# Kernel tuning notes

Measured on AMD Instinct MI355X. Metric: run time of the kernel, lower is better.

The kernel has to match this reference:

```python
import jax, jax.numpy as jnp
import numpy as np

T_STEPS = 64   # number of actions (T-1 in the torch code)
BATCH = 512
STATE = 256
ACTION = 64
BELIEF = 1024
HIDDEN = 1024
EMB = 1024
MIN_STD = 0.1


def setup_inputs() -> dict:
    key = jax.random.key(0)
    ks = jax.random.split(key, 16)
    def w(k, shape):
        return jax.random.normal(k, shape, jnp.float32) * 0.02
    return {
        "s_0": jax.random.normal(ks[0], (BATCH, STATE), jnp.float32),
        "A": jax.random.normal(ks[1], (T_STEPS, BATCH, ACTION), jnp.float32),
        "b_0": jax.random.normal(ks[2], (BATCH, BELIEF), jnp.float32),
        "O": jax.random.normal(ks[3], (T_STEPS, BATCH, EMB), jnp.float32),
        "M": jnp.ones((T_STEPS, BATCH, 1), jnp.float32),
        "noise_pri": jax.random.normal(ks[4], (T_STEPS, BATCH, STATE), jnp.float32),
        "noise_pos": jax.random.normal(ks[5], (T_STEPS, BATCH, STATE), jnp.float32),
        # learned parameters (torch nn.Linear convention: y = x @ W.T + b)
        "W_sa": w(ks[6], (BELIEF, STATE + ACTION)), "b_sa": jnp.zeros((BELIEF,), jnp.float32),
        "W_ih": w(ks[7], (3 * BELIEF, BELIEF)), "b_ih": jnp.zeros((3 * BELIEF,), jnp.float32),
        "W_hh": w(ks[8], (3 * BELIEF, BELIEF)), "b_hh": jnp.zeros((3 * BELIEF,), jnp.float32),
        "W_bpri": w(ks[9], (HIDDEN, BELIEF)), "b_bpri": jnp.zeros((HIDDEN,), jnp.float32),
        "W_spri": w(ks[10], (2 * STATE, HIDDEN)), "b_spri": jnp.zeros((2 * STATE,), jnp.float32),
        "W_bpos": w(ks[11], (HIDDEN, BELIEF + EMB)), "b_bpos": jnp.zeros((HIDDEN,), jnp.float32),
        "W_spos": w(ks[12], (2 * STATE, HIDDEN)), "b_spos": jnp.zeros((2 * STATE,), jnp.float32),
    }


def reference(s_0, A, b_0, O, M, noise_pri, noise_pos,
              W_sa, b_sa, W_ih, b_ih, W_hh, b_hh,
              W_bpri, b_bpri, W_spri, b_spri,
              W_bpos, b_bpos, W_spos, b_spos):
    act = jax.nn.relu  # cfg.activation_function = 'relu'

    def gru_cell(x, h):
        # torch GRUCell gate order: r, z, n
        gi = x @ W_ih.T + b_ih      # [B, 3*BELIEF]
        gh = h @ W_hh.T + b_hh
        i_r, i_z, i_n = jnp.split(gi, 3, axis=1)
        h_r, h_z, h_n = jnp.split(gh, 3, axis=1)
        r = jax.nn.sigmoid(i_r + h_r)
        z = jax.nn.sigmoid(i_z + h_z)
        n = jnp.tanh(i_n + r * h_n)
        return (1.0 - z) * n + z * h

    def step(carry, xs):
        b, s = carry  # belief [B,BELIEF], posterior state [B,STATE]
        a_t, o_t, m_t, eps_p, eps_q = xs
        s_in = s * m_t  # non-terminal mask
        x = act(jnp.concatenate([s_in, a_t], axis=1) @ W_sa.T + b_sa)
        b_new = gru_cell(x, b)
        # prior
        pri = act(b_new @ W_bpri.T + b_bpri) @ W_spri.T + b_spri
        mu_p, hp = jnp.split(pri, 2, axis=1)
        std_p = jax.nn.softplus(hp) + MIN_STD
        s_p = mu_p + std_p * eps_p
        # posterior (uses current observation embedding)
        pos = act(jnp.concatenate([b_new, o_t], axis=1) @ W_bpos.T + b_bpos) @ W_spos.T + b_spos
        mu_q, hq = jnp.split(pos, 2, axis=1)
        std_q = jax.nn.softplus(hq) + MIN_STD
        s_q = mu_q + std_q * eps_q
        return (b_new, s_q), (b_new, s_p, mu_p, std_p, s_q, mu_q, std_q)

    (_, _), ys = jax.lax.scan(step, (b_0, s_0), (A, O, M, noise_pri, noise_pos))
    B_out, S_pri, MU_pri, STD_pri, S_pos, MU_pos, STD_pos = ys
    return B_out, S_pri, MU_pri, STD_pri, S_pos, MU_pos, STD_pos
```

## Files before the change

kernel.cpp:

```cpp
#include <hip/hip_runtime.h>
#include <hip/hip_bf16.h>
#include <math.h>

typedef short bf16x8 __attribute__((ext_vector_type(8)));
typedef float f32x4 __attribute__((ext_vector_type(4)));
typedef unsigned short u16;

#define NT 64
#define NB 512
#define NS 256
#define NA 64
#define NBEL 1024

#define OUT_B      0
#define OUT_SPRI   33554432
#define OUT_MUPRI  41943040
#define OUT_STDPRI 50331648
#define OUT_SPOS   58720256
#define OUT_MUPOS  67108864
#define OUT_STDPOS 75497472

__device__ __forceinline__ f32x4 mfma16(bf16x8 a, bf16x8 b, f32x4 c) {
  return __builtin_amdgcn_mfma_f32_16x16x32_bf16(a, b, c, 0, 0, 0);
}

__device__ __forceinline__ u16 f2bf(float f) {
  union { float f; unsigned u; } v; v.f = f;
  return (u16)((v.u + 0x7FFFu + ((v.u >> 16) & 1u)) >> 16);
}
__device__ __forceinline__ float bf2f(u16 h) {
  union { unsigned u; float f; } v; v.u = ((unsigned)h) << 16; return v.f;
}

__device__ __forceinline__ bf16x8 ld8bf(const u16* p) { return *(const bf16x8*)p; }

__device__ __forceinline__ bf16x8 cvt8(const float* p) {
  const float4 lo = *(const float4*)p;
  const float4 hi = *(const float4*)(p + 4);
  bf16x8 v;
  v[0] = (short)f2bf(lo.x); v[1] = (short)f2bf(lo.y);
  v[2] = (short)f2bf(lo.z); v[3] = (short)f2bf(lo.w);
  v[4] = (short)f2bf(hi.x); v[5] = (short)f2bf(hi.y);
  v[6] = (short)f2bf(hi.z); v[7] = (short)f2bf(hi.w);
  return v;
}

__device__ __forceinline__ float sigm(float x) { return 1.f / (1.f + __expf(-x)); }
__device__ __forceinline__ float softplus_(float x) {
  if (x > 20.f) return x;
  return log1pf(__expf(x));
}

#define ZACC(acc) { acc[0][0] = (f32x4){0.f,0.f,0.f,0.f}; acc[0][1] = (f32x4){0.f,0.f,0.f,0.f}; \
                    acc[1][0] = (f32x4){0.f,0.f,0.f,0.f}; acc[1][1] = (f32x4){0.f,0.f,0.f,0.f}; }

#define Q4(acc, a0v, a1v, b0v, b1v) \
  acc[0][0] = mfma16(a0v, b0v, acc[0][0]); \
  acc[0][1] = mfma16(a0v, b1v, acc[0][1]); \
  acc[1][0] = mfma16(a1v, b0v, acc[1][0]); \
  acc[1][1] = mfma16(a1v, b1v, acc[1][1]);

__device__ __forceinline__ void gtile(f32x4 (&acc)[2][2],
    const u16* __restrict__ A, int lda, const u16* __restrict__ B, int ldb,
    int K, int r16, int kq) {
  const u16* A0 = A + r16 * lda + kq * 8;
  const u16* A1 = A0 + 16 * lda;
  const u16* B0 = B + (size_t)r16 * ldb + kq * 8;
  const u16* B1 = B0 + 16 * ldb;
#pragma unroll 4
  for (int k = 0; k < K; k += 32) {
    bf16x8 a0 = ld8bf(A0 + k), a1 = ld8bf(A1 + k);
    bf16x8 b0 = ld8bf(B0 + k), b1 = ld8bf(B1 + k);
    Q4(acc, a0, a1, b0, b1);
  }
}
__device__ __forceinline__ void gtileF(f32x4 (&acc)[2][2],
    const float* __restrict__ A, int lda, const u16* __restrict__ B, int ldb,
    int K, int r16, int kq) {
  const float* A0 = A + r16 * lda + kq * 8;
  const float* A1 = A0 + 16 * lda;
  const u16* B0 = B + (size_t)r16 * ldb + kq * 8;
  const u16* B1 = B0 + 16 * ldb;
#pragma unroll 2
  for (int k = 0; k < K; k += 32) {
    bf16x8 a0 = cvt8(A0 + k), a1 = cvt8(A1 + k);
    bf16x8 b0 = ld8bf(B0 + k), b1 = ld8bf(B1 + k);
    Q4(acc, a0, a1, b0, b1);
  }
}

__device__ __forceinline__ void red_write(float* L, f32x4 (&acc)[2][2], int l) {
  const int base = l * 16;
#pragma unroll
  for (int i = 0; i < 2; ++i)
#pragma unroll
    for (int j = 0; j < 2; ++j)
#pragma unroll
      for (int q = 0; q < 4; ++q)
        L[base + (i * 2 + j) * 4 + q] = acc[i][j][q];
}
__device__ __forceinline__ void red_add(const float* L, f32x4 (&acc)[2][2], int l) {
  const int base = l * 16;
#pragma unroll
  for (int i = 0; i < 2; ++i)
#pragma unroll
    for (int j = 0; j < 2; ++j)
#pragma unroll
      for (int q = 0; q < 4; ++q)
        acc[i][j][q] += L[base + (i * 2 + j) * 4 + q];
}

__device__ __forceinline__ void setflag_blk(unsigned* f) {
  __syncthreads();
  if (threadIdx.x == 0)
    __hip_atomic_fetch_add(f, 1u, __ATOMIC_RELEASE, __HIP_MEMORY_SCOPE_AGENT);
}
__device__ __forceinline__ void waitflag_blk(unsigned* f, unsigned target) {
  if (threadIdx.x == 0) {
    while (__hip_atomic_load(f, __ATOMIC_RELAXED, __HIP_MEMORY_SCOPE_AGENT) < target)
      __builtin_amdgcn_s_sleep(2);
    (void)__hip_atomic_load(f, __ATOMIC_ACQUIRE, __HIP_MEMORY_SCOPE_AGENT);
  }
  __syncthreads();
}

__global__ __launch_bounds__(256) void cvt_weights_k(
    const float* __restrict__ wsa, const float* __restrict__ wih,
    const float* __restrict__ whh, const float* __restrict__ wbpri,
    const float* __restrict__ wspri, const float* __restrict__ wbpos,
    const float* __restrict__ wspos, u16* __restrict__ dst) {
  const int S0 = 327680;
  const int S1 = S0 + 3145728;
  const int S2 = S1 + 3145728;
  const int S3 = S2 + 1048576;
  const int S4 = S3 + 524288;
  const int S5 = S4 + 2097152;
  const int S6 = S5 + 524288;
  for (int i = blockIdx.x * blockDim.x + threadIdx.x; i < S6;
       i += gridDim.x * blockDim.x) {
    float v;
    if (i < S0) v = wsa[i];
    else if (i < S1) v = wih[i - S0];
    else if (i < S2) v = whh[i - S1];
    else if (i < S3) v = wbpri[i - S2];
    else if (i < S4) v = wspri[i - S3];
    else if (i < S5) v = wbpos[i - S4];
    else v = wspos[i - S5];
    dst[i] = f2bf(v);
  }
}

__global__ __launch_bounds__(256) void init_carry_k(
    const float* __restrict__ s0, const float* __restrict__ b0,
    const float* __restrict__ Mptr, u16* __restrict__ smask,
    u16* __restrict__ bbf, float* __restrict__ hf,
    unsigned* __restrict__ flags) {
  for (int i = blockIdx.x * blockDim.x + threadIdx.x; i < NB * NBEL;
       i += gridDim.x * blockDim.x) {
    float b = b0[i];
    bbf[i] = f2bf(b);
    hf[i] = b;
    if (i < NB * NS) {
      int row = i >> 8;
      smask[i] = f2bf(s0[i] * Mptr[row]);
    }
    if (i < 3 * NT) flags[i] = 0;
  }
}


__device__ __forceinline__ void dev_spri(
    int g, int wid, int kh, int r16, int kq, int l, int tt,
    const u16* __restrict__ hpri, const u16* __restrict__ wspri,
    const float* __restrict__ bspri, const float* __restrict__ npri,
    float* __restrict__ out, float* lred0, float* lred1) {
  const int bm = g >> 2, bn = g & 3;
  const int row0 = bm * 64 + (wid >> 1) * 32;
  const int c0 = bn * 64 + (wid & 1) * 32;
  f32x4 am[2][2], ah[2][2];
  ZACC(am); ZACC(ah);
  const u16* A0 = hpri + (row0 + r16) * NBEL + kh * 512 + kq * 8;
  const u16* A1 = A0 + 16 * NBEL;
  const u16* Bm0 = wspri + (size_t)(c0 + r16) * NBEL + kh * 512 + kq * 8;
  const u16* Bm1 = Bm0 + 16 * NBEL;
  const u16* Bh0 = wspri + (size_t)(c0 + 256 + r16) * NBEL + kh * 512 + kq * 8;
  const u16* Bh1 = Bh0 + 16 * NBEL;
#pragma unroll 4
  for (int k = 0; k < 512; k += 32) {
    bf16x8 a0 = ld8bf(A0 + k), a1 = ld8bf(A1 + k);
    bf16x8 m0 = ld8bf(Bm0 + k), m1 = ld8bf(Bm1 + k);
    Q4(am, a0, a1, m0, m1);
    bf16x8 h0 = ld8bf(Bh0 + k), h1 = ld8bf(Bh1 + k);
    Q4(ah, a0, a1, h0, h1);
  }
  if (kh == 1) {
    red_write(lred0, am, l);
    red_write(lred1, ah, l);
  }
  __syncthreads();
  if (kh == 0) {
    red_add(lred0, am, l);
    red_add(lred1, ah, l);
#pragma unroll
    for (int i = 0; i < 2; ++i)
#pragma unroll
      for (int j = 0; j < 2; ++j)
#pragma unroll
        for (int q = 0; q < 4; ++q) {
          const int row = row0 + i * 16 + kq * 4 + q;
          const int c = c0 + j * 16 + r16;
          const size_t idx = (size_t)tt * (NB * NS) + (size_t)row * NS + c;
          const float mu = am[i][j][q] + bspri[c];
          const float hp = ah[i][j][q] + bspri[c + 256];
          const float sd = softplus_(hp) + 0.1f;
          out[OUT_SPRI + idx] = mu + sd * npri[idx];
          out[OUT_MUPRI + idx] = mu;
          out[OUT_STDPRI + idx] = sd;
        }
  }
}

__device__ __forceinline__ void dev_x64(
    int g, int wid8, int r16, int kq, int t,
    const u16* __restrict__ smask, const float* __restrict__ Af,
    const u16* __restrict__ wsa, const float* __restrict__ bsa,
    u16* __restrict__ xg) {
  const int row0 = (g >> 3) * 64 + (wid8 >> 2) * 32;
  const int col0 = (g & 7) * 128 + (wid8 & 3) * 32;
  f32x4 acc[2][2]; ZACC(acc);
  gtile(acc, smask + row0 * NS, NS, wsa + (size_t)col0 * 320, 320, 256, r16, kq);
  gtileF(acc, Af + (size_t)t * (NB * NA) + (size_t)row0 * NA, NA,
         wsa + (size_t)col0 * 320 + 256, 320, 64, r16, kq);
#pragma unroll
  for (int i = 0; i < 2; ++i)
#pragma unroll
    for (int j = 0; j < 2; ++j)
#pragma unroll
      for (int q = 0; q < 4; ++q) {
        const int row = row0 + i * 16 + kq * 4 + q;
        const int col = col0 + j * 16 + r16;
        xg[row * NBEL + col] = f2bf(fmaxf(acc[i][j][q] + bsa[col], 0.f));
      }
}

__device__ __forceinline__ void dev_hbO64(
    int g, int wid8, int r16, int kq,
    const float* __restrict__ OfT, const u16* __restrict__ wbpos,
    float* __restrict__ hbOn) {
  const int row0 = (g >> 3) * 64 + (wid8 >> 2) * 32;
  const int col0 = (g & 7) * 128 + (wid8 & 3) * 32;
  f32x4 acc[2][2]; ZACC(acc);
  gtileF(acc, OfT + (size_t)row0 * NBEL, NBEL,
         wbpos + (size_t)col0 * 2048 + 1024, 2048, 1024, r16, kq);
#pragma unroll
  for (int i = 0; i < 2; ++i)
#pragma unroll
    for (int j = 0; j < 2; ++j)
#pragma unroll
      for (int q = 0; q < 4; ++q) {
        const int row = row0 + i * 16 + kq * 4 + q;
        const int col = col0 + j * 16 + r16;
        hbOn[row * NBEL + col] = acc[i][j][q];
      }
}

__device__ __forceinline__ void dev_gh96(
    int g, int wid8, int r16, int kq,
    const u16* __restrict__ bsrc, const u16* __restrict__ whh,
    const float* __restrict__ bhh, u16* __restrict__ ghn) {
  const int bm = g / 12, bc = g % 12;
  const int row0 = bm * 64 + (wid8 >> 2) * 32;
#pragma unroll
  for (int jt = 0; jt < 2; ++jt) {
    const int col0 = bc * 256 + (wid8 & 3) * 32 + jt * 128;
    f32x4 acc[2][2]; ZACC(acc);
    gtile(acc, bsrc + row0 * NBEL, NBEL, whh + (size_t)col0 * NBEL, NBEL,
          1024, r16, kq);
#pragma unroll
    for (int i = 0; i < 2; ++i)
#pragma unroll
      for (int j = 0; j < 2; ++j)
#pragma unroll
        for (int q = 0; q < 4; ++q) {
          const int row = row0 + i * 16 + kq * 4 + q;
          const int col = col0 + j * 16 + r16;
          ghn[row * 3072 + col] = f2bf(acc[i][j][q] + bhh[col]);
        }
  }
}

__device__ __forceinline__ void dev_bpri64(
    int g, int wid8, int r16, int kq,
    const u16* __restrict__ bcur, const u16* __restrict__ wbpri,
    const float* __restrict__ bbpri, u16* __restrict__ hpri) {
  const int row0 = (g >> 3) * 64 + (wid8 >> 2) * 32;
  const int col0 = (g & 7) * 128 + (wid8 & 3) * 32;
  f32x4 acc[2][2]; ZACC(acc);
  gtile(acc, bcur + row0 * NBEL, NBEL, wbpri + (size_t)col0 * NBEL, NBEL,
        1024, r16, kq);
#pragma unroll
  for (int i = 0; i < 2; ++i)
#pragma unroll
    for (int j = 0; j < 2; ++j)
#pragma unroll
      for (int q = 0; q < 4; ++q) {
        const int row = row0 + i * 16 + kq * 4 + q;
        const int col = col0 + j * 16 + r16;
        hpri[row * NBEL + col] = f2bf(fmaxf(acc[i][j][q] + bbpri[col], 0.f));
      }
}

__global__ __launch_bounds__(512, 2) void kX0(
    const u16* __restrict__ smask, const float* __restrict__ Af,
    const u16* __restrict__ wsa, const float* __restrict__ bsa,
    u16* __restrict__ xg, const float* __restrict__ Of,
    const u16* __restrict__ wbpos, float* __restrict__ hbO0,
    const u16* __restrict__ bbf, const u16* __restrict__ whh,
    const float* __restrict__ bhh, u16* __restrict__ ghA) {
  const int l = threadIdx.x & 63, r16 = l & 15, kq = l >> 4;
  const int wid8 = threadIdx.x >> 6;
  if (blockIdx.x < 64) {
    dev_x64(blockIdx.x, wid8, r16, kq, 0, smask, Af, wsa, bsa, xg);
  } else if (blockIdx.x < 128) {
    dev_hbO64(blockIdx.x - 64, wid8, r16, kq, Of, wbpos, hbO0);
  } else {
    dev_gh96(blockIdx.x - 128, wid8, r16, kq, bbf, whh, bhh, ghA);
  }
}

__global__ __launch_bounds__(512, 2) void kG(
    const u16* __restrict__ xg, const u16* __restrict__ wih,
    const float* __restrict__ bih, const u16* __restrict__ ghc,
    float* __restrict__ hf, u16* __restrict__ bcur, float* __restrict__ out,
    const u16* __restrict__ hpri, const u16* __restrict__ wspri,
    const float* __restrict__ bspri, const float* __restrict__ npri, int t) {
  __shared__ float lred[4][3][1024];
  const int l = threadIdx.x & 63, r16 = l & 15, kq = l >> 4;
  const int wid8 = threadIdx.x >> 6;
  const int wid = wid8 & 3, kh = wid8 >> 2;
  if (blockIdx.x < 128) {
    const int g = blockIdx.x, bm = g >> 4, bn = g & 15;
    const int row0 = bm * 64 + (wid >> 1) * 32;
    const int col0 = bn * 64 + (wid & 1) * 32;
    f32x4 ar[2][2], az[2][2], an[2][2];
    ZACC(ar); ZACC(az); ZACC(an);
    const u16* A0 = xg + (row0 + r16) * NBEL + kh * 512 + kq * 8;
    const u16* A1 = A0 + 16 * NBEL;
    const u16* Br0 = wih + (size_t)(col0 + r16) * NBEL + kh * 512 + kq * 8;
    const u16* Br1 = Br0 + 16 * NBEL;
    const u16* Bz0 = wih + (size_t)(col0 + 1024 + r16) * NBEL + kh * 512 + kq * 8;
    const u16* Bz1 = Bz0 + 16 * NBEL;
    const u16* Bn0 = wih + (size_t)(col0 + 2048 + r16) * NBEL + kh * 512 + kq * 8;
    const u16* Bn1 = Bn0 + 16 * NBEL;
#pragma unroll 4
    for (int k = 0; k < 512; k += 32) {
      bf16x8 a0 = ld8bf(A0 + k), a1 = ld8bf(A1 + k);
      bf16x8 b0 = ld8bf(Br0 + k), b1 = ld8bf(Br1 + k);
      Q4(ar, a0, a1, b0, b1);
      bf16x8 c0 = ld8bf(Bz0 + k), c1 = ld8bf(Bz1 + k);
      Q4(az, a0, a1, c0, c1);
      bf16x8 d0 = ld8bf(Bn0 + k), d1 = ld8bf(Bn1 + k);
      Q4(an, a0, a1, d0, d1);
    }
    if (kh == 1) {
      red_write(&lred[wid][0][0], ar, l);
      red_write(&lred[wid][1][0], az, l);
      red_write(&lred[wid][2][0], an, l);
    }
    __syncthreads();
    if (kh == 0) {
      const int base = l * 16;
#pragma unroll
      for (int i = 0; i < 2; ++i)
#pragma unroll
        for (int j = 0; j < 2; ++j)
#pragma unroll
          for (int q = 0; q < 4; ++q) {
            const int row = row0 + i * 16 + kq * 4 + q;
            const int c = col0 + j * 16 + r16;
            const int li = base + (i * 2 + j) * 4 + q;
            const u16* ghrow = ghc + row * 3072;
            const float r = sigm(ar[i][j][q] + lred[wid][0][li] + bih[c] +
                                 bf2f(ghrow[c]));
            const float z = sigm(az[i][j][q] + lred[wid][1][li] + bih[c + 1024] +
                                 bf2f(ghrow[c + 1024]));
            const float n = tanhf(an[i][j][q] + lred[wid][2][li] + bih[c + 2048] +
                                  r * bf2f(ghrow[c + 2048]));
            const float h = hf[row * NBEL + c];
            const float bnew = (1.f - z) * n + z * h;
            hf[row * NBEL + c] = bnew;
            bcur[row * NBEL + c] = f2bf(bnew);
            out[OUT_B + (size_t)t * (NB * NBEL) + row * NBEL + c] = bnew;
          }
    }
  } else if (t >= 1) {
    dev_spri(blockIdx.x - 128, wid, kh, r16, kq, l, t - 1,
             hpri, wspri, bspri, npri, out,
             &lred[wid][0][0], &lred[wid][1][0]);
  }
}

__global__ __launch_bounds__(512, 2) void kM(
    const u16* __restrict__ bcur, const u16* __restrict__ wbpos,
    const float* __restrict__ bbpos, const float* __restrict__ hbOc,
    u16* __restrict__ hbbf,
    const u16* __restrict__ wbpri, const float* __restrict__ bbpri,
    u16* __restrict__ hpri,
    const u16* __restrict__ whh, const float* __restrict__ bhh,
    u16* __restrict__ ghn,
    const float* __restrict__ Of, float* __restrict__ hbOn,
    const u16* __restrict__ wspos, const float* __restrict__ bspos,
    const float* __restrict__ npos, const float* __restrict__ Mptr,
    u16* __restrict__ smask,
    const float* __restrict__ Af, const u16* __restrict__ wsa,
    const float* __restrict__ bsa, u16* __restrict__ xg,
    const u16* __restrict__ wspri, const float* __restrict__ bspri,
    const float* __restrict__ npri,
    float* __restrict__ out,
    unsigned* __restrict__ fH, unsigned* __restrict__ fS,
    unsigned* __restrict__ fB, int t) {
  __shared__ float lred[4][2][1024];
  const int l = threadIdx.x & 63, r16 = l & 15, kq = l >> 4;
  const int wid8 = threadIdx.x >> 6;
  const int wid = wid8 & 3, kh = wid8 >> 2;
  if (blockIdx.x < 128) {
    const int g = blockIdx.x, bm = g >> 4, bn = g & 15;
    const int row0 = bm * 64 + (wid >> 1) * 32;
    const int col0 = bn * 64 + (wid & 1) * 32;
    f32x4 acc[2][2]; ZACC(acc);
    const u16* A0 = bcur + (row0 + r16) * NBEL + kh * 512 + kq * 8;
    const u16* A1 = A0 + 16 * NBEL;
    const u16* B0 = wbpos + (size_t)(col0 + r16) * 2048 + kh * 512 + kq * 8;
    const u16* B1 = B0 + 16 * 2048;
#pragma unroll 4
    for (int k = 0; k < 512; k += 32) {
      bf16x8 a0 = ld8bf(A0 + k), a1 = ld8bf(A1 + k);
      bf16x8 b0 = ld8bf(B0 + k), b1 = ld8bf(B1 + k);
      Q4(acc, a0, a1, b0, b1);
    }
    if (kh == 1) red_write(&lred[wid][0][0], acc, l);
    __syncthreads();
    if (kh == 0) {
      red_add(&lred[wid][0][0], acc, l);
#pragma unroll
      for (int i = 0; i < 2; ++i)
#pragma unroll
        for (int j = 0; j < 2; ++j)
#pragma unroll
          for (int q = 0; q < 4; ++q) {
            const int row = row0 + i * 16 + kq * 4 + q;
            const int col = col0 + j * 16 + r16;
            const float v = acc[i][j][q] + hbOc[row * NBEL + col] + bbpos[col];
            hbbf[row * NBEL + col] = f2bf(fmaxf(v, 0.f));
          }
    }
    setflag_blk(&fH[t]);
  } else if (blockIdx.x < 192) {
    dev_bpri64(blockIdx.x - 128, wid8, r16, kq, bcur, wbpri, bbpri, hpri);
    setflag_blk(&fB[t]);
  } else if (blockIdx.x < 288) {
    if (t + 1 >= NT) return;
    dev_gh96(blockIdx.x - 192, wid8, r16, kq, bcur, whh, bhh, ghn);
  } else if (blockIdx.x < 352) {
    if (t + 1 >= NT) return;
    dev_hbO64(blockIdx.x - 288, wid8, r16, kq,
              Of + (size_t)(t + 1) * (NB * NBEL), wbpos, hbOn);
  } else if (blockIdx.x < 384) {
    waitflag_blk(&fH[t], 128);
    const int g = blockIdx.x - 352, bm = g >> 2, bn = g & 3;
    const int row0 = bm * 64 + (wid >> 1) * 32;
    const int c0 = bn * 64 + (wid & 1) * 32;
    f32x4 am[2][2], ah[2][2];
    ZACC(am); ZACC(ah);
    const u16* A0 = hbbf + (row0 + r16) * NBEL + kh * 512 + kq * 8;
    const u16* A1 = A0 + 16 * NBEL;
    const u16* Bm0 = wspos + (size_t)(c0 + r16) * NBEL + kh * 512 + kq * 8;
    const u16* Bm1 = Bm0 + 16 * NBEL;
    const u16* Bh0 = wspos + (size_t)(c0 + 256 + r16) * NBEL + kh * 512 + kq * 8;
    const u16* Bh1 = Bh0 + 16 * NBEL;
#pragma unroll 4
    for (int k = 0; k < 512; k += 32) {
      bf16x8 a0 = ld8bf(A0 + k), a1 = ld8bf(A1 + k);
      bf16x8 m0 = ld8bf(Bm0 + k), m1 = ld8bf(Bm1 + k);
      Q4(am, a0, a1, m0, m1);
      bf16x8 h0 = ld8bf(Bh0 + k), h1 = ld8bf(Bh1 + k);
      Q4(ah, a0, a1, h0, h1);
    }
    if (kh == 1) {
      red_write(&lred[wid][0][0], am, l);
      red_write(&lred[wid][1][0], ah, l);
    }
    __syncthreads();
    if (kh == 0) {
      red_add(&lred[wid][0][0], am, l);
      red_add(&lred[wid][1][0], ah, l);
#pragma unroll
      for (int i = 0; i < 2; ++i)
#pragma unroll
        for (int j = 0; j < 2; ++j)
#pragma unroll
          for (int q = 0; q < 4; ++q) {
            const int row = row0 + i * 16 + kq * 4 + q;
            const int c = c0 + j * 16 + r16;
            const float mu = am[i][j][q] + bspos[c];
            const float hq = ah[i][j][q] + bspos[c + 256];
            const float sd = softplus_(hq) + 0.1f;
            const size_t idx = (size_t)t * (NB * NS) + (size_t)row * NS + c;
            const float sq = mu + sd * npos[idx];
            out[OUT_SPOS + idx] = sq;
            out[OUT_MUPOS + idx] = mu;
            out[OUT_STDPOS + idx] = sd;
            const float mn = (t < NT - 1) ? Mptr[(t + 1) * NB + row] : 1.f;
            smask[row * NS + c] = f2bf(sq * mn);
          }
    }
    setflag_blk(&fS[t]);
  } else if (blockIdx.x < 448) {
    if (t + 1 >= NT) return;
    waitflag_blk(&fS[t], 32);
    dev_x64(blockIdx.x - 384, wid8, r16, kq, t + 1, smask, Af, wsa, bsa, xg);
  } else {
    if (t != NT - 1) return;
    waitflag_blk(&fB[t], 64);
    dev_spri(blockIdx.x - 448, wid, kh, r16, kq, l, t,
             hpri, wspri, bspri, npri, out,
             &lred[wid][0][0], &lred[wid][1][0]);
  }
}

extern "C" void kernel_launch(void* const* d_in, const int* in_sizes, int n_in,
                              void* d_out, int out_size, void* d_ws, size_t ws_size,
                              hipStream_t stream) {
  const float* s0 = (const float*)d_in[0];
  const float* Af = (const float*)d_in[1];
  const float* b0 = (const float*)d_in[2];
  const float* Of = (const float*)d_in[3];
  const float* Mp = (const float*)d_in[4];
  const float* npri = (const float*)d_in[5];
  const float* npos = (const float*)d_in[6];
  const float* Wsa = (const float*)d_in[7];
  const float* bsa = (const float*)d_in[8];
  const float* Wih = (const float*)d_in[9];
  const float* bih = (const float*)d_in[10];
  const float* Whh = (const float*)d_in[11];
  const float* bhh = (const float*)d_in[12];
  const float* Wbpri = (const float*)d_in[13];
  const float* bbpri = (const float*)d_in[14];
  const float* Wspri = (const float*)d_in[15];
  const float* bspri = (const float*)d_in[16];
  const float* Wbpos = (const float*)d_in[17];
  const float* bbpos = (const float*)d_in[18];
  const float* Wspos = (const float*)d_in[19];
  const float* bspos = (const float*)d_in[20];

  float* out = (float*)d_out;
  char* ws = (char*)d_ws;
  u16* wbase   = (u16*)ws;
  u16* wsa_b   = wbase;
  u16* wih_b   = wbase + 327680;
  u16* whh_b   = wbase + 3473408;
  u16* wbpri_b = wbase + 6619136;
  u16* wspri_b = wbase + 7667712;
  u16* wbpos_b = wbase + 8192000;
  u16* wspos_b = wbase + 10289152;
  u16*   smask = (u16*)  (ws + 21626880);
  u16*   bbf   = (u16*)  (ws + 21889024);
  float* hf    = (float*)(ws + 22937600);
  u16*   xg    = (u16*)  (ws + 25034752);
  float* hbO0  = (float*)(ws + 26083328);
  float* hbO1  = (float*)(ws + 28180480);
  u16*   hbbf  = (u16*)  (ws + 30277632);
  u16*   hpri  = (u16*)  (ws + 31326208);
  u16*   ghA   = (u16*)  (ws + 32374784);
  u16*   ghB   = (u16*)  (ws + 35520512);
  unsigned* flags = (unsigned*)(ws + 38666240);
  unsigned* fH = flags, *fS = flags + NT, *fB = flags + 2 * NT;

  cvt_weights_k<<<2048, 256, 0, stream>>>(Wsa, Wih, Whh, Wbpri, Wspri, Wbpos,
                                          Wspos, wbase);
  init_carry_k<<<2048, 256, 0, stream>>>(s0, b0, Mp, smask, bbf, hf, flags);
  kX0<<<224, 512, 0, stream>>>(smask, Af, wsa_b, bsa, xg, Of, wbpos_b, hbO0,
                               bbf, whh_b, bhh, ghA);

  for (int t = 0; t < NT; ++t) {
    float* hbOc = (t & 1) ? hbO1 : hbO0;
    float* hbOn = (t & 1) ? hbO0 : hbO1;
    u16* ghc = (t & 1) ? ghB : ghA;
    u16* ghn = (t & 1) ? ghA : ghB;
    kG<<<160, 512, 0, stream>>>(xg, wih_b, bih, ghc, hf, bbf, out,
                                hpri, wspri_b, bspri, npri, t);
    kM<<<480, 512, 0, stream>>>(bbf, wbpos_b, bbpos, hbOc, hbbf,
                                wbpri_b, bbpri, hpri,
                                whh_b, bhh, ghn,
                                Of, hbOn,
                                wspos_b, bspos, npos, Mp, smask,
                                Af, wsa_b, bsa, xg,
                                wspri_b, bspri, npri,
                                out, fH, fS, fB, t);
  }
}
```

Baseline: 8.208 ms.

## Merge per-step GRU and head kernels into one flag-synchronized kernel

Folds the two per-timestep launches (GRU gate kernel and the multi-stage head kernel) into a single 496-block launch. Blocks coordinate through global flags: a new GRU-done flag gates the posterior, prior-hidden and next-step W_hh projections. The prior-hidden buffer is double-buffered so the delayed prior-state head can read the previous step while the current one is written. The W_hh, prior-hidden and observation-projection stages now run on fewer, larger blocks to fit the combined grid. This removes one launch boundary per step and lets independent stages overlap with the GRU tail, at the cost of spin-waiting blocks that rely on every block being resident at once.

```diff
diff --git a/kernel.cpp b/kernel.cpp
--- a/kernel.cpp
+++ b/kernel.cpp
@@ -164,7 +164,7 @@
       int row = i >> 8;
       smask[i] = f2bf(s0[i] * Mptr[row]);
     }
-    if (i < 3 * NT) flags[i] = 0;
+    if (i < 4 * NT) flags[i] = 0;
   }
 }
 
@@ -264,6 +264,30 @@
       }
 }
 
+__device__ __forceinline__ void dev_hbO32(
+    int g, int wid8, int r16, int kq,
+    const float* __restrict__ OfT, const u16* __restrict__ wbpos,
+    float* __restrict__ hbOn) {
+  const int row0 = (g >> 2) * 64 + (wid8 >> 2) * 32;
+#pragma unroll
+  for (int jt = 0; jt < 2; ++jt) {
+    const int col0 = (g & 3) * 256 + jt * 128 + (wid8 & 3) * 32;
+    f32x4 acc[2][2]; ZACC(acc);
+    gtileF(acc, OfT + (size_t)row0 * NBEL, NBEL,
+           wbpos + (size_t)col0 * 2048 + 1024, 2048, 1024, r16, kq);
+#pragma unroll
+    for (int i = 0; i < 2; ++i)
+#pragma unroll
+      for (int j = 0; j < 2; ++j)
+#pragma unroll
+        for (int q = 0; q < 4; ++q) {
+          const int row = row0 + i * 16 + kq * 4 + q;
+          const int col = col0 + j * 16 + r16;
+          hbOn[row * NBEL + col] = acc[i][j][q];
+        }
+  }
+}
+
 __device__ __forceinline__ void dev_gh96(
     int g, int wid8, int r16, int kq,
     const u16* __restrict__ bsrc, const u16* __restrict__ whh,
@@ -289,25 +313,53 @@
   }
 }
 
-__device__ __forceinline__ void dev_bpri64(
+__device__ __forceinline__ void dev_gh48(
+    int g, int wid8, int r16, int kq,
+    const u16* __restrict__ bsrc, const u16* __restrict__ whh,
+    const float* __restrict__ bhh, u16* __restrict__ ghn) {
+  const int bm = g / 6, bc = g % 6;
+  const int row0 = bm * 64 + (wid8 >> 2) * 32;
+#pragma unroll
+  for (int jt = 0; jt < 4; ++jt) {
+    const int col0 = bc * 512 + jt * 128 + (wid8 & 3) * 32;
+    f32x4 acc[2][2]; ZACC(acc);
+    gtile(acc, bsrc + row0 * NBEL, NBEL, whh + (size_t)col0 * NBEL, NBEL,
+          1024, r16, kq);
+#pragma unroll
+    for (int i = 0; i < 2; ++i)
+#pragma unroll
+      for (int j = 0; j < 2; ++j)
+#pragma unroll
+        for (int q = 0; q < 4; ++q) {
+          const int row = row0 + i * 16 + kq * 4 + q;
+          const int col = col0 + j * 16 + r16;
+          ghn[row * 3072 + col] = f2bf(acc[i][j][q] + bhh[col]);
+        }
+  }
+}
+
+__device__ __forceinline__ void dev_bpri32(
     int g, int wid8, int r16, int kq,
     const u16* __restrict__ bcur, const u16* __restrict__ wbpri,
     const float* __restrict__ bbpri, u16* __restrict__ hpri) {
-  const int row0 = (g >> 3) * 64 + (wid8 >> 2) * 32;
-  const int col0 = (g & 7) * 128 + (wid8 & 3) * 32;
-  f32x4 acc[2][2]; ZACC(acc);
-  gtile(acc, bcur + row0 * NBEL, NBEL, wbpri + (size_t)col0 * NBEL, NBEL,
-        1024, r16, kq);
-#pragma unroll
-  for (int i = 0; i < 2; ++i)
-#pragma unroll
-    for (int j = 0; j < 2; ++j)
-#pragma unroll
-      for (int q = 0; q < 4; ++q) {
-        const int row = row0 + i * 16 + kq * 4 + q;
-        const int col = col0 + j * 16 + r16;
-        hpri[row * NBEL + col] = f2bf(fmaxf(acc[i][j][q] + bbpri[col], 0.f));
-      }
+  const int row0 = (g >> 2) * 64 + (wid8 >> 2) * 32;
+#pragma unroll
+  for (int jt = 0; jt < 2; ++jt) {
+    const int col0 = (g & 3) * 256 + jt * 128 + (wid8 & 3) * 32;
+    f32x4 acc[2][2]; ZACC(acc);
+    gtile(acc, bcur + row0 * NBEL, NBEL, wbpri + (size_t)col0 * NBEL, NBEL,
+          1024, r16, kq);
+#pragma unroll
+    for (int i = 0; i < 2; ++i)
+#pragma unroll
+      for (int j = 0; j < 2; ++j)
+#pragma unroll
+        for (int q = 0; q < 4; ++q) {
+          const int row = row0 + i * 16 + kq * 4 + q;
+          const int col = col0 + j * 16 + r16;
+          hpri[row * NBEL + col] = f2bf(fmaxf(acc[i][j][q] + bbpri[col], 0.f));
+        }
+  }
 }
 
 __global__ __launch_bounds__(512, 2) void kX0(
@@ -328,12 +380,26 @@
   }
 }
 
-__global__ __launch_bounds__(512, 2) void kG(
+__global__ __launch_bounds__(512, 2) void kS(
     const u16* __restrict__ xg, const u16* __restrict__ wih,
     const float* __restrict__ bih, const u16* __restrict__ ghc,
-    float* __restrict__ hf, u16* __restrict__ bcur, float* __restrict__ out,
-    const u16* __restrict__ hpri, const u16* __restrict__ wspri,
-    const float* __restrict__ bspri, const float* __restrict__ npri, int t) {
+    float* __restrict__ hf, u16* __restrict__ bbf, float* __restrict__ out,
+    const u16* __restrict__ hpriPrev, u16* __restrict__ hpriCur,
+    const u16* __restrict__ wspri, const float* __restrict__ bspri,
+    const float* __restrict__ npri,
+    const u16* __restrict__ wbpos, const float* __restrict__ bbpos,
+    const float* __restrict__ hbOc, u16* __restrict__ hbbf,
+    const u16* __restrict__ wbpri, const float* __restrict__ bbpri,
+    const u16* __restrict__ whh, const float* __restrict__ bhh,
+    u16* __restrict__ ghn,
+    const float* __restrict__ Of, float* __restrict__ hbOn,
+    const u16* __restrict__ wspos, const float* __restrict__ bspos,
+    const float* __restrict__ npos, const float* __restrict__ Mptr,
+    u16* __restrict__ smask,
+    const float* __restrict__ Af, const u16* __restrict__ wsa,
+    const float* __restrict__ bsa,
+    unsigned* __restrict__ fG, unsigned* __restrict__ fH,
+    unsigned* __restrict__ fS, unsigned* __restrict__ fB, int t) {
   __shared__ float lred[4][3][1024];
   const int l = threadIdx.x & 63, r16 = l & 15, kq = l >> 4;
   const int wid8 = threadIdx.x >> 6;
@@ -389,46 +455,23 @@
             const float h = hf[row * NBEL + c];
             const float bnew = (1.f - z) * n + z * h;
             hf[row * NBEL + c] = bnew;
-            bcur[row * NBEL + c] = f2bf(bnew);
+            bbf[row * NBEL + c] = f2bf(bnew);
             out[OUT_B + (size_t)t * (NB * NBEL) + row * NBEL + c] = bnew;
           }
     }
-  } else if (t >= 1) {
-    dev_spri(blockIdx.x - 128, wid, kh, r16, kq, l, t - 1,
-             hpri, wspri, bspri, npri, out,
-             &lred[wid][0][0], &lred[wid][1][0]);
-  }
-}
-
-__global__ __launch_bounds__(512, 2) void kM(
-    const u16* __restrict__ bcur, const u16* __restrict__ wbpos,
-    const float* __restrict__ bbpos, const float* __restrict__ hbOc,
-    u16* __restrict__ hbbf,
-    const u16* __restrict__ wbpri, const float* __restrict__ bbpri,
-    u16* __restrict__ hpri,
-    const u16* __restrict__ whh, const float* __restrict__ bhh,
-    u16* __restrict__ ghn,
-    const float* __restrict__ Of, float* __restrict__ hbOn,
-    const u16* __restrict__ wspos, const float* __restrict__ bspos,
-    const float* __restrict__ npos, const float* __restrict__ Mptr,
-    u16* __restrict__ smask,
-    const float* __restrict__ Af, const u16* __restrict__ wsa,
-    const float* __restrict__ bsa, u16* __restrict__ xg,
-    const u16* __restrict__ wspri, const float* __restrict__ bspri,
-    const float* __restrict__ npri,
-    float* __restrict__ out,
-    unsigned* __restrict__ fH, unsigned* __restrict__ fS,
-    unsigned* __restrict__ fB, int t) {
-  __shared__ float lred[4][2][1024];
-  const int l = threadIdx.x & 63, r16 = l & 15, kq = l >> 4;
-  const int wid8 = threadIdx.x >> 6;
-  const int wid = wid8 & 3, kh = wid8 >> 2;
-  if (blockIdx.x < 128) {
-    const int g = blockIdx.x, bm = g >> 4, bn = g & 15;
+    setflag_blk(fG + t);
+  } else if (blockIdx.x < 160) {
+    if (t >= 1)
+      dev_spri(blockIdx.x - 128, wid, kh, r16, kq, l, t - 1,
+               hpriPrev, wspri, bspri, npri, out,
+               &lred[wid][0][0], &lred[wid][1][0]);
+  } else if (blockIdx.x < 288) {
+    waitflag_blk(fG + t, 128);
+    const int g = blockIdx.x - 160, bm = g >> 4, bn = g & 15;
     const int row0 = bm * 64 + (wid >> 1) * 32;
     const int col0 = bn * 64 + (wid & 1) * 32;
     f32x4 acc[2][2]; ZACC(acc);
-    const u16* A0 = bcur + (row0 + r16) * NBEL + kh * 512 + kq * 8;
+    const u16* A0 = bbf + (row0 + r16) * NBEL + kh * 512 + kq * 8;
     const u16* A1 = A0 + 16 * NBEL;
     const u16* B0 = wbpos + (size_t)(col0 + r16) * 2048 + kh * 512 + kq * 8;
     const u16* B1 = B0 + 16 * 2048;
@@ -454,20 +497,23 @@
             hbbf[row * NBEL + col] = f2bf(fmaxf(v, 0.f));
           }
     }
-    setflag_blk(&fH[t]);
-  } else if (blockIdx.x < 192) {
-    dev_bpri64(blockIdx.x - 128, wid8, r16, kq, bcur, wbpri, bbpri, hpri);
-    setflag_blk(&fB[t]);
-  } else if (blockIdx.x < 288) {
-    if (t + 1 >= NT) return;
-    dev_gh96(blockIdx.x - 192, wid8, r16, kq, bcur, whh, bhh, ghn);
-  } else if (blockIdx.x < 352) {
-    if (t + 1 >= NT) return;
-    dev_hbO64(blockIdx.x - 288, wid8, r16, kq,
-              Of + (size_t)(t + 1) * (NB * NBEL), wbpos, hbOn);
-  } else if (blockIdx.x < 384) {
-    waitflag_blk(&fH[t], 128);
-    const int g = blockIdx.x - 352, bm = g >> 2, bn = g & 3;
+    setflag_blk(fH + t);
+  } else if (blockIdx.x < 320) {
+    waitflag_blk(fG + t, 128);
+    dev_bpri32(blockIdx.x - 288, wid8, r16, kq, bbf, wbpri, bbpri, hpriCur);
+    setflag_blk(fB + t);
+  } else if (blockIdx.x < 368) {
+    if (t + 1 < NT) {
+      waitflag_blk(fG + t, 128);
+      dev_gh48(blockIdx.x - 320, wid8, r16, kq, bbf, whh, bhh, ghn);
+    }
+  } else if (blockIdx.x < 400) {
+    if (t + 1 < NT)
+      dev_hbO32(blockIdx.x - 368, wid8, r16, kq,
+                Of + (size_t)(t + 1) * (NB * NBEL), wbpos, hbOn);
+  } else if (blockIdx.x < 432) {
+    waitflag_blk(fH + t, 128);
+    const int g = blockIdx.x - 400, bm = g >> 2, bn = g & 3;
     const int row0 = bm * 64 + (wid >> 1) * 32;
     const int c0 = bn * 64 + (wid & 1) * 32;
     f32x4 am[2][2], ah[2][2];
@@ -514,17 +560,18 @@
             smask[row * NS + c] = f2bf(sq * mn);
           }
     }
-    setflag_blk(&fS[t]);
-  } else if (blockIdx.x < 448) {
-    if (t + 1 >= NT) return;
-    waitflag_blk(&fS[t], 32);
-    dev_x64(blockIdx.x - 384, wid8, r16, kq, t + 1, smask, Af, wsa, bsa, xg);
+    setflag_blk(fS + t);
   } else {
-    if (t != NT - 1) return;
-    waitflag_blk(&fB[t], 64);
-    dev_spri(blockIdx.x - 448, wid, kh, r16, kq, l, t,
-             hpri, wspri, bspri, npri, out,
-             &lred[wid][0][0], &lred[wid][1][0]);
+    if (t + 1 < NT) {
+      waitflag_blk(fS + t, 32);
+      dev_x64(blockIdx.x - 432, wid8, r16, kq, t + 1, smask, Af, wsa, bsa,
+              (u16*)xg);
+    } else if (blockIdx.x < 464) {
+      waitflag_blk(fB + t, 32);
+      dev_spri(blockIdx.x - 432, wid, kh, r16, kq, l, t,
+               hpriCur, wspri, bspri, npri, out,
+               &lred[wid][0][0], &lred[wid][1][0]);
+    }
   }
 }
 
@@ -570,11 +617,13 @@
   float* hbO0  = (float*)(ws + 26083328);
   float* hbO1  = (float*)(ws + 28180480);
   u16*   hbbf  = (u16*)  (ws + 30277632);
-  u16*   hpri  = (u16*)  (ws + 31326208);
-  u16*   ghA   = (u16*)  (ws + 32374784);
-  u16*   ghB   = (u16*)  (ws + 35520512);
-  unsigned* flags = (unsigned*)(ws + 38666240);
-  unsigned* fH = flags, *fS = flags + NT, *fB = flags + 2 * NT;
+  u16*   hpri0 = (u16*)  (ws + 31326208);
+  u16*   hpri1 = (u16*)  (ws + 32374784);
+  u16*   ghA   = (u16*)  (ws + 33423360);
+  u16*   ghB   = (u16*)  (ws + 36569088);
+  unsigned* flags = (unsigned*)(ws + 39714816);
+  unsigned* fG = flags, *fH = flags + NT, *fS = flags + 2 * NT,
+          *fB = flags + 3 * NT;
 
   cvt_weights_k<<<2048, 256, 0, stream>>>(Wsa, Wih, Whh, Wbpri, Wspri, Wbpos,
                                           Wspos, wbase);
@@ -587,15 +636,16 @@
     float* hbOn = (t & 1) ? hbO0 : hbO1;
     u16* ghc = (t & 1) ? ghB : ghA;
     u16* ghn = (t & 1) ? ghA : ghB;
-    kG<<<160, 512, 0, stream>>>(xg, wih_b, bih, ghc, hf, bbf, out,
-                                hpri, wspri_b, bspri, npri, t);
-    kM<<<480, 512, 0, stream>>>(bbf, wbpos_b, bbpos, hbOc, hbbf,
-                                wbpri_b, bbpri, hpri,
+    u16* hpriCur  = (t & 1) ? hpri1 : hpri0;
+    u16* hpriPrev = (t & 1) ? hpri0 : hpri1;
+    kS<<<496, 512, 0, stream>>>(xg, wih_b, bih, ghc, hf, bbf, out,
+                                hpriPrev, hpriCur, wspri_b, bspri, npri,
+                                wbpos_b, bbpos, hbOc, hbbf,
+                                wbpri_b, bbpri,
                                 whh_b, bhh, ghn,
                                 Of, hbOn,
                                 wspos_b, bspos, npos, Mp, smask,
-                                Af, wsa_b, bsa, xg,
-                                wspri_b, bspri, npri,
-                                out, fH, fS, fB, t);
-  }
-}
+                                Af, wsa_b, bsa,
+                                fG, fH, fS, fB, t);
+  }
+}
```

Result: slower. 14.18 ms (+72.8%).

## Move next-step obs projection into GRU kernel and use per-row-block flags

Applied to the files above, without the earlier changes.

The O_{t+1}·W_bpos projection for the next step moves from the kM kernel into the kG kernel as extra blocks, so it runs alongside the GRU gate GEMM. kM shrinks from 480 to 416 blocks. The single global flags become per-row-block flags, so each posterior block waits only for its 16 producer blocks and each x-projection block waits only for its 4. The prior hidden buffer is double-buffered so kG at step t can read step t-1's hpri while kM writes the new one. The aim is to fill idle CUs in the underoccupied kG launch and to cut spin-wait latency, at the cost of more grid blocks and more flag bookkeeping.

```diff
diff --git a/kernel.cpp b/kernel.cpp
--- a/kernel.cpp
+++ b/kernel.cpp
@@ -164,7 +164,7 @@
       int row = i >> 8;
       smask[i] = f2bf(s0[i] * Mptr[row]);
     }
-    if (i < 3 * NT) flags[i] = 0;
+    if (i < 2048) flags[i] = 0;
   }
 }
 
@@ -332,8 +332,10 @@
     const u16* __restrict__ xg, const u16* __restrict__ wih,
     const float* __restrict__ bih, const u16* __restrict__ ghc,
     float* __restrict__ hf, u16* __restrict__ bcur, float* __restrict__ out,
-    const u16* __restrict__ hpri, const u16* __restrict__ wspri,
-    const float* __restrict__ bspri, const float* __restrict__ npri, int t) {
+    const u16* __restrict__ hpriPrev, const u16* __restrict__ wspri,
+    const float* __restrict__ bspri, const float* __restrict__ npri,
+    const float* __restrict__ Of, const u16* __restrict__ wbpos,
+    float* __restrict__ hbOn, int t) {
   __shared__ float lred[4][3][1024];
   const int l = threadIdx.x & 63, r16 = l & 15, kq = l >> 4;
   const int wid8 = threadIdx.x >> 6;
@@ -393,10 +395,15 @@
             out[OUT_B + (size_t)t * (NB * NBEL) + row * NBEL + c] = bnew;
           }
     }
-  } else if (t >= 1) {
-    dev_spri(blockIdx.x - 128, wid, kh, r16, kq, l, t - 1,
-             hpri, wspri, bspri, npri, out,
-             &lred[wid][0][0], &lred[wid][1][0]);
+  } else if (blockIdx.x < 160) {
+    if (t >= 1)
+      dev_spri(blockIdx.x - 128, wid, kh, r16, kq, l, t - 1,
+               hpriPrev, wspri, bspri, npri, out,
+               &lred[wid][0][0], &lred[wid][1][0]);
+  } else {
+    if (t + 1 < NT)
+      dev_hbO64(blockIdx.x - 160, wid8, r16, kq,
+                Of + (size_t)(t + 1) * (NB * NBEL), wbpos, hbOn);
   }
 }
 
@@ -405,10 +412,9 @@
     const float* __restrict__ bbpos, const float* __restrict__ hbOc,
     u16* __restrict__ hbbf,
     const u16* __restrict__ wbpri, const float* __restrict__ bbpri,
-    u16* __restrict__ hpri,
+    u16* __restrict__ hpriCur,
     const u16* __restrict__ whh, const float* __restrict__ bhh,
     u16* __restrict__ ghn,
-    const float* __restrict__ Of, float* __restrict__ hbOn,
     const u16* __restrict__ wspos, const float* __restrict__ bspos,
     const float* __restrict__ npos, const float* __restrict__ Mptr,
     u16* __restrict__ smask,
@@ -417,7 +423,7 @@
     const u16* __restrict__ wspri, const float* __restrict__ bspri,
     const float* __restrict__ npri,
     float* __restrict__ out,
-    unsigned* __restrict__ fH, unsigned* __restrict__ fS,
+    unsigned* __restrict__ fH8, unsigned* __restrict__ fS8,
     unsigned* __restrict__ fB, int t) {
   __shared__ float lred[4][2][1024];
   const int l = threadIdx.x & 63, r16 = l & 15, kq = l >> 4;
@@ -454,20 +460,16 @@
             hbbf[row * NBEL + col] = f2bf(fmaxf(v, 0.f));
           }
     }
-    setflag_blk(&fH[t]);
+    setflag_blk(fH8 + t * 8 + bm);
   } else if (blockIdx.x < 192) {
-    dev_bpri64(blockIdx.x - 128, wid8, r16, kq, bcur, wbpri, bbpri, hpri);
-    setflag_blk(&fB[t]);
+    dev_bpri64(blockIdx.x - 128, wid8, r16, kq, bcur, wbpri, bbpri, hpriCur);
+    setflag_blk(fB + t);
   } else if (blockIdx.x < 288) {
-    if (t + 1 >= NT) return;
-    dev_gh96(blockIdx.x - 192, wid8, r16, kq, bcur, whh, bhh, ghn);
-  } else if (blockIdx.x < 352) {
-    if (t + 1 >= NT) return;
-    dev_hbO64(blockIdx.x - 288, wid8, r16, kq,
-              Of + (size_t)(t + 1) * (NB * NBEL), wbpos, hbOn);
-  } else if (blockIdx.x < 384) {
-    waitflag_blk(&fH[t], 128);
-    const int g = blockIdx.x - 352, bm = g >> 2, bn = g & 3;
+    if (t + 1 < NT)
+      dev_gh96(blockIdx.x - 192, wid8, r16, kq, bcur, whh, bhh, ghn);
+  } else if (blockIdx.x < 320) {
+    const int g = blockIdx.x - 288, bm = g >> 2, bn = g & 3;
+    waitflag_blk(fH8 + t * 8 + bm, 16);
     const int row0 = bm * 64 + (wid >> 1) * 32;
     const int c0 = bn * 64 + (wid & 1) * 32;
     f32x4 am[2][2], ah[2][2];
@@ -514,16 +516,17 @@
             smask[row * NS + c] = f2bf(sq * mn);
           }
     }
-    setflag_blk(&fS[t]);
-  } else if (blockIdx.x < 448) {
+    setflag_blk(fS8 + t * 8 + bm);
+  } else if (blockIdx.x < 384) {
     if (t + 1 >= NT) return;
-    waitflag_blk(&fS[t], 32);
-    dev_x64(blockIdx.x - 384, wid8, r16, kq, t + 1, smask, Af, wsa, bsa, xg);
+    const int g = blockIdx.x - 320;
+    waitflag_blk(fS8 + t * 8 + (g >> 3), 4);
+    dev_x64(g, wid8, r16, kq, t + 1, smask, Af, wsa, bsa, xg);
   } else {
     if (t != NT - 1) return;
-    waitflag_blk(&fB[t], 64);
-    dev_spri(blockIdx.x - 448, wid, kh, r16, kq, l, t,
-             hpri, wspri, bspri, npri, out,
+    waitflag_blk(fB + t, 64);
+    dev_spri(blockIdx.x - 384, wid, kh, r16, kq, l, t,
+             hpriCur, wspri, bspri, npri, out,
              &lred[wid][0][0], &lred[wid][1][0]);
   }
 }
@@ -570,11 +573,14 @@
   float* hbO0  = (float*)(ws + 26083328);
   float* hbO1  = (float*)(ws + 28180480);
   u16*   hbbf  = (u16*)  (ws + 30277632);
-  u16*   hpri  = (u16*)  (ws + 31326208);
-  u16*   ghA   = (u16*)  (ws + 32374784);
-  u16*   ghB   = (u16*)  (ws + 35520512);
-  unsigned* flags = (unsigned*)(ws + 38666240);
-  unsigned* fH = flags, *fS = flags + NT, *fB = flags + 2 * NT;
+  u16*   hpri0 = (u16*)  (ws + 31326208);
+  u16*   hpri1 = (u16*)  (ws + 32374784);
+  u16*   ghA   = (u16*)  (ws + 33423360);
+  u16*   ghB   = (u16*)  (ws + 36569088);
+  unsigned* flags = (unsigned*)(ws + 39714816);
+  unsigned* fH8 = flags;
+  unsigned* fS8 = flags + 512;
+  unsigned* fB  = flags + 1024;
 
   cvt_weights_k<<<2048, 256, 0, stream>>>(Wsa, Wih, Whh, Wbpri, Wspri, Wbpos,
                                           Wspos, wbase);
@@ -587,15 +593,17 @@
     float* hbOn = (t & 1) ? hbO0 : hbO1;
     u16* ghc = (t & 1) ? ghB : ghA;
     u16* ghn = (t & 1) ? ghA : ghB;
-    kG<<<160, 512, 0, stream>>>(xg, wih_b, bih, ghc, hf, bbf, out,
-                                hpri, wspri_b, bspri, npri, t);
-    kM<<<480, 512, 0, stream>>>(bbf, wbpos_b, bbpos, hbOc, hbbf,
-                                wbpri_b, bbpri, hpri,
+    u16* hpriCur  = (t & 1) ? hpri1 : hpri0;
+    u16* hpriPrev = (t & 1) ? hpri0 : hpri1;
+    kG<<<224, 512, 0, stream>>>(xg, wih_b, bih, ghc, hf, bbf, out,
+                                hpriPrev, wspri_b, bspri, npri,
+                                Of, wbpos_b, hbOn, t);
+    kM<<<416, 512, 0, stream>>>(bbf, wbpos_b, bbpos, hbOc, hbbf,
+                                wbpri_b, bbpri, hpriCur,
                                 whh_b, bhh, ghn,
-                                Of, hbOn,
                                 wspos_b, bspos, npos, Mp, smask,
                                 Af, wsa_b, bsa, xg,
                                 wspri_b, bspri, npri,
-                                out, fH, fS, fB, t);
-  }
-}
+                                out, fH8, fS8, fB, t);
+  }
+}
```

Measured after the change: 8.095 ms (median of 2 runs). About the same (-1.4%).
